# Kernel optimization log

Hardware: AMD Instinct MI355X
Metric: run time of the kernel (lower is better)

Reference implementation:

```python
import jax, jax.numpy as jnp
import numpy as np

HIDDEN = 128
NI = 100000   # ingredient nodes
NT = 100000   # taste nodes
E = 800000    # part_of edges
EPS = 1e-5


def setup_inputs() -> dict:
    key = jax.random.key(0)
    ks = jax.random.split(key, 12)
    s = 1.0 / np.sqrt(HIDDEN)
    return {
        "x_ingredient": jax.random.normal(ks[0], (NI, HIDDEN), jnp.float32),
        "x_taste": jax.random.normal(ks[1], (NT, HIDDEN), jnp.float32),
        "edge_index": jax.random.randint(ks[2], (2, E), 0, 100000, jnp.int64),
        "W_ing": jax.random.normal(ks[3], (HIDDEN, HIDDEN), jnp.float32) * s,
        "b_ing": jax.random.normal(ks[4], (HIDDEN,), jnp.float32) * s,
        "W_taste": jax.random.normal(ks[5], (HIDDEN, HIDDEN), jnp.float32) * s,
        "b_taste": jax.random.normal(ks[6], (HIDDEN,), jnp.float32) * s,
        "att_src": jax.random.normal(ks[7], (HIDDEN,), jnp.float32) * s,
        "att_dst": jax.random.normal(ks[8], (HIDDEN,), jnp.float32) * s,
        "k_lin_W": jax.random.normal(ks[9], (HIDDEN, HIDDEN), jnp.float32) * s,
        "k_lin_b": jax.random.normal(ks[10], (HIDDEN,), jnp.float32) * s,
        "q": jax.random.normal(ks[11], (HIDDEN,), jnp.float32) * s,
        "gamma": jnp.ones((HIDDEN,), jnp.float32),
        "beta": jnp.zeros((HIDDEN,), jnp.float32),
    }


def reference(x_ingredient, x_taste, edge_index, W_ing, b_ing, W_taste, b_taste,
              att_src, att_dst, k_lin_W, k_lin_b, q, gamma, beta):
    # Per-node-type linear projection (HANConv, heads=1)
    h_src = x_ingredient @ W_ing.T + b_ing      # [NI, D]
    h_dst = x_taste @ W_taste.T + b_taste       # [NT, D]

    # Per-node attention logits
    a_src = h_src @ att_src                     # [NI]
    a_dst = h_dst @ att_dst                     # [NT]

    src, dst = edge_index[0], edge_index[1]
    alpha = jax.nn.leaky_relu(a_src[src] + a_dst[dst], negative_slope=0.2)  # [E]

    # Segment softmax over incoming edges of each taste node
    m = jax.ops.segment_max(alpha, dst, num_segments=NT)
    m = jnp.where(jnp.isfinite(m), m, 0.0)      # empty segments -> 0
    e = jnp.exp(alpha - m[dst])
    denom = jax.ops.segment_sum(e, dst, num_segments=NT)
    coef = e / jnp.where(denom[dst] == 0, 1.0, denom[dst])  # [E]

    # Weighted scatter-add aggregation, then per-metapath ReLU (as in HANConv)
    agg = jax.ops.segment_sum(coef[:, None] * h_src[src], dst, num_segments=NT)  # [NT, D]
    agg = jax.nn.relu(agg)

    # Semantic attention across metapaths (single metapath -> weight 1.0)
    w = jnp.tanh(agg @ k_lin_W.T + k_lin_b).mean(0) @ q     # scalar
    beta_sem = jax.nn.softmax(w[None])[0]                   # == 1.0
    out = beta_sem * agg

    # BatchNorm (training statistics) + ReLU
    mu = out.mean(0)
    var = out.var(0)
    out = (out - mu) / jnp.sqrt(var + EPS) * gamma + beta
    return jax.nn.relu(out)
```

## Files before the change

kernel.cpp:

```cpp
#include <hip/hip_runtime.h>
#include <hip/hip_bf16.h>

#define HIDDEN 128
#define NI_N 100000
#define NT_N 100000
#define NE_N 800000
#define EPS_F 1e-5f
#define ELLW 32
#define STATS_B 512

#define NB_PROJ 782
#define NB_SC 512
#define SC_THREADS (NB_SC * 256)
#define SC_K 7
#define NB_ADST 3125
#define NB_ZERO 391

typedef __attribute__((ext_vector_type(8))) short bf16x8;
typedef __attribute__((ext_vector_type(4))) float f32x4;

static __device__ __forceinline__ unsigned short f2bf(float f) {
  unsigned u = __float_as_uint(f);
  u += 0x7FFFu + ((u >> 16) & 1u);
  return (unsigned short)(u >> 16);
}

static __device__ __forceinline__ bf16x8 pack8(float4 a, float4 b) {
  bf16x8 r;
  r[0] = (short)f2bf(a.x); r[1] = (short)f2bf(a.y);
  r[2] = (short)f2bf(a.z); r[3] = (short)f2bf(a.w);
  r[4] = (short)f2bf(b.x); r[5] = (short)f2bf(b.y);
  r[6] = (short)f2bf(b.z); r[7] = (short)f2bf(b.w);
  return r;
}

static __device__ __forceinline__ float bf_lo(unsigned int h) {
  return __uint_as_float(h << 16);
}
static __device__ __forceinline__ float bf_hi(unsigned int h) {
  return __uint_as_float(h & 0xffff0000u);
}


__global__ __launch_bounds__(256) void k_pre(const float* __restrict__ W,
                                             const float* __restrict__ b,
                                             const float* __restrict__ att,
                                             float* __restrict__ wbuf,
                                             int* __restrict__ cursor) {
  int bid = blockIdx.x, t = threadIdx.x;
  if (bid < NB_ZERO) {
    int i = bid * 256 + t;
    if (i < NT_N) cursor[i] = 0;
    return;
  }
  __shared__ float red[128];
  if (t < 128) {
    float s = 0.f;
#pragma unroll 8
    for (int c = 0; c < 128; ++c) s += att[c] * W[c * 128 + t];
    wbuf[t] = s;
    red[t] = att[t] * b[t];
  }
  __syncthreads();
  if (t < 64) {
    float v = red[t] + red[t + 64];
    v += __shfl_xor(v, 1);
    v += __shfl_xor(v, 2);
    v += __shfl_xor(v, 4);
    v += __shfl_xor(v, 8);
    v += __shfl_xor(v, 16);
    v += __shfl_xor(v, 32);
    if (t == 0) wbuf[128] = v;
  }
}

__global__ __launch_bounds__(256) void k_main(
    const float* __restrict__ x, const float* __restrict__ W,
    const float* __restrict__ bias, const float* __restrict__ att,
    unsigned int* __restrict__ h32, float* __restrict__ a_src,
    const int* __restrict__ esrc, const int* __restrict__ edst,
    int* __restrict__ cursor, int* __restrict__ ell,
    const float* __restrict__ xt, const float* __restrict__ wbuf,
    float* __restrict__ a_dst) {
  const int t = threadIdx.x;

  if (blockIdx.x >= NB_PROJ && blockIdx.x < NB_PROJ + NB_SC) {
    int base = (blockIdx.x - NB_PROJ) * 256 + t;
    int sv[SC_K], dv[SC_K];
    bool ok[SC_K];
#pragma unroll
    for (int k = 0; k < SC_K; ++k) {
      int e = base + k * SC_THREADS;
      ok[k] = e < NE_N;
      int ec = ok[k] ? e : (NE_N - 1);
      sv[k] = esrc[ec];
      dv[k] = edst[ec];
    }
#pragma unroll
    for (int k = 0; k < SC_K; ++k) {
      if (ok[k]) {
        int pos = atomicAdd(&cursor[dv[k]], 1);
        if (pos < ELLW) ell[dv[k] * ELLW + pos] = sv[k];
      }
    }
    return;
  }

  if (blockIdx.x >= NB_PROJ + NB_SC) {
    __shared__ float swe[128];
    if (t < 128) swe[t] = wbuf[t];
    __syncthreads();
    float be = wbuf[128];
    int lane = t & 63, wv = t >> 6;
    int sub = lane & 7, r = lane >> 3;
    int node = (blockIdx.x - NB_PROJ - NB_SC) * 32 + wv * 8 + r;
    if (node >= NT_N) return;
    const float* xp = xt + (size_t)node * 128 + sub * 4;
    float4 v0 = *(const float4*)(xp);
    float4 v1 = *(const float4*)(xp + 32);
    float4 v2 = *(const float4*)(xp + 64);
    float4 v3 = *(const float4*)(xp + 96);
    const float* wp = swe + sub * 4;
    float4 w0 = *(const float4*)(wp);
    float4 w1 = *(const float4*)(wp + 32);
    float4 w2 = *(const float4*)(wp + 64);
    float4 w3 = *(const float4*)(wp + 96);
    float s = v0.x * w0.x + v0.y * w0.y + v0.z * w0.z + v0.w * w0.w;
    s += v1.x * w1.x + v1.y * w1.y + v1.z * w1.z + v1.w * w1.w;
    s += v2.x * w2.x + v2.y * w2.y + v2.z * w2.z + v2.w * w2.w;
    s += v3.x * w3.x + v3.y * w3.y + v3.z * w3.z + v3.w * w3.w;
    s += __shfl_xor(s, 1);
    s += __shfl_xor(s, 2);
    s += __shfl_xor(s, 4);
    if (sub == 0) a_dst[node] = s + be;
    return;
  }

  const int bid = blockIdx.x;
  __shared__ float sh_a[128];
  if (t < 128) sh_a[t] = 0.f;
  __syncthreads();

  const int wave = t >> 6, lane = t & 63;
  const int colhalf = wave & 1, rowhalf = wave >> 1;
  const int row0 = bid * 128 + rowhalf * 64;
  const int lr = lane & 15;
  const int q = lane >> 4;

  bf16x8 bfrag[4][4];
  float bv[4], av[4];
#pragma unroll
  for (int nt = 0; nt < 4; ++nt) {
    int wrow = colhalf * 64 + nt * 16 + lr;
    const float* wp = W + wrow * 128 + q * 8;
#pragma unroll
    for (int kb = 0; kb < 4; ++kb) {
      float4 wa = *(const float4*)(wp + kb * 32);
      float4 wb = *(const float4*)(wp + kb * 32 + 4);
      bfrag[nt][kb] = pack8(wa, wb);
    }
    bv[nt] = bias[wrow];
    av[nt] = att[wrow];
  }

#pragma unroll
  for (int rt = 0; rt < 4; ++rt) {
    int arow = row0 + rt * 16 + lr;
    int rowc = (arow < NI_N) ? arow : (NI_N - 1);
    const float* xp = x + (size_t)rowc * 128 + q * 8;
    bf16x8 afrag[4];
#pragma unroll
    for (int kb = 0; kb < 4; ++kb) {
      float4 xa = *(const float4*)(xp + kb * 32);
      float4 xb = *(const float4*)(xp + kb * 32 + 4);
      afrag[kb] = pack8(xa, xb);
    }
    float part[4] = {0.f, 0.f, 0.f, 0.f};
    f32x4 cc[4];
#pragma unroll
    for (int nt = 0; nt < 4; ++nt) {
      f32x4 c = {0.f, 0.f, 0.f, 0.f};
#pragma unroll
      for (int kb = 0; kb < 4; ++kb)
        c = __builtin_amdgcn_mfma_f32_16x16x32_bf16(afrag[kb], bfrag[nt][kb], c,
                                                    0, 0, 0);
#pragma unroll
      for (int i = 0; i < 4; ++i) {
        float v = c[i] + bv[nt];
        part[i] += v * av[nt];
        c[i] = v;
      }
      cc[nt] = c;
    }
#pragma unroll
    for (int i = 0; i < 4; ++i) {
      int orow = row0 + rt * 16 + q * 4 + i;
      if (orow < NI_N) {
        unsigned u0 = (unsigned)f2bf(cc[0][i]) | ((unsigned)f2bf(cc[1][i]) << 16);
        unsigned u1 = (unsigned)f2bf(cc[2][i]) | ((unsigned)f2bf(cc[3][i]) << 16);
        unsigned int* hp = h32 + (size_t)orow * 64 + colhalf * 32 + lr;
        hp[0] = u0;
        hp[16] = u1;
      }
      float p = part[i];
      p += __shfl_xor(p, 1);
      p += __shfl_xor(p, 2);
      p += __shfl_xor(p, 4);
      p += __shfl_xor(p, 8);
      if (lr == 0)
        atomicAdd(&sh_a[rowhalf * 64 + rt * 16 + q * 4 + i], p);
    }
  }
  __syncthreads();
  if (t < 128) {
    int row = bid * 128 + t;
    if (row < NI_N) a_src[row] = sh_a[t];
  }
}

__global__ __launch_bounds__(256) void k_agg(const int* __restrict__ deg,
                                             const int* __restrict__ ell,
                                             const float* __restrict__ a_src,
                                             const float* __restrict__ a_dst,
                                             const unsigned int* __restrict__ h32,
                                             unsigned int* __restrict__ aggb) {
  int wv = (blockIdx.x * blockDim.x + threadIdx.x) >> 6;
  int lane = threadIdx.x & 63;
  int half = lane >> 5, l = lane & 31;
  int node = wv * 2 + half;
  if (node >= NT_N) return;
  int n = deg[node];
  n = (n > ELLW) ? ELLW : n;
  float ax = 0.f, ay = 0.f, bx = 0.f, by = 0.f;
  if (n > 0) {
    float ad = a_dst[node];
    int li = (l < n) ? l : (n - 1);
    int sr = ell[node * ELLW + li];
    float al = a_src[sr] + ad;
    al = (al > 0.f) ? al : 0.2f * al;
    float ex = (l < n) ? __expf(al) : 0.f;
    float den = 0.f;
    const int sb = half << 5;
    int n8 = (n + 7) & ~7;
    const uint2* h2 = (const uint2*)h32;
    for (int j = 0; j < n8; j += 8) {
      int s0 = __shfl(sr, sb + j + 0), s1 = __shfl(sr, sb + j + 1);
      int s2 = __shfl(sr, sb + j + 2), s3 = __shfl(sr, sb + j + 3);
      int s4 = __shfl(sr, sb + j + 4), s5 = __shfl(sr, sb + j + 5);
      int s6 = __shfl(sr, sb + j + 6), s7 = __shfl(sr, sb + j + 7);
      float e0 = __shfl(ex, sb + j + 0), e1 = __shfl(ex, sb + j + 1);
      float e2 = __shfl(ex, sb + j + 2), e3 = __shfl(ex, sb + j + 3);
      float e4 = __shfl(ex, sb + j + 4), e5 = __shfl(ex, sb + j + 5);
      float e6 = __shfl(ex, sb + j + 6), e7 = __shfl(ex, sb + j + 7);
      uint2 g0 = h2[s0 * 32 + l];
      uint2 g1 = h2[s1 * 32 + l];
      uint2 g2 = h2[s2 * 32 + l];
      uint2 g3 = h2[s3 * 32 + l];
      uint2 g4 = h2[s4 * 32 + l];
      uint2 g5 = h2[s5 * 32 + l];
      uint2 g6 = h2[s6 * 32 + l];
      uint2 g7 = h2[s7 * 32 + l];
      ax += e0 * bf_lo(g0.x) + e1 * bf_lo(g1.x) + e2 * bf_lo(g2.x) +
            e3 * bf_lo(g3.x) + e4 * bf_lo(g4.x) + e5 * bf_lo(g5.x) +
            e6 * bf_lo(g6.x) + e7 * bf_lo(g7.x);
      ay += e0 * bf_hi(g0.x) + e1 * bf_hi(g1.x) + e2 * bf_hi(g2.x) +
            e3 * bf_hi(g3.x) + e4 * bf_hi(g4.x) + e5 * bf_hi(g5.x) +
            e6 * bf_hi(g6.x) + e7 * bf_hi(g7.x);
      bx += e0 * bf_lo(g0.y) + e1 * bf_lo(g1.y) + e2 * bf_lo(g2.y) +
            e3 * bf_lo(g3.y) + e4 * bf_lo(g4.y) + e5 * bf_lo(g5.y) +
            e6 * bf_lo(g6.y) + e7 * bf_lo(g7.y);
      by += e0 * bf_hi(g0.y) + e1 * bf_hi(g1.y) + e2 * bf_hi(g2.y) +
            e3 * bf_hi(g3.y) + e4 * bf_hi(g4.y) + e5 * bf_hi(g5.y) +
            e6 * bf_hi(g6.y) + e7 * bf_hi(g7.y);
      den += ((e0 + e1) + (e2 + e3)) + ((e4 + e5) + (e6 + e7));
    }
    float inv = 1.f / den;
    ax *= inv; ay *= inv; bx *= inv; by *= inv;
  }
  ax = fmaxf(ax, 0.f);
  ay = fmaxf(ay, 0.f);
  bx = fmaxf(bx, 0.f);
  by = fmaxf(by, 0.f);
  uint2 o;
  o.x = (unsigned)f2bf(ax) | ((unsigned)f2bf(ay) << 16);
  o.y = (unsigned)f2bf(bx) | ((unsigned)f2bf(by) << 16);
  ((uint2*)aggb)[node * 32 + l] = o;
}

__global__ __launch_bounds__(256) void k_stats1(const unsigned int* __restrict__ aggb,
                                                float* __restrict__ partials) {
  __shared__ float red[4][64][4];
  int t = threadIdx.x;
  int p = t & 63, g = t >> 6;
  float sl = 0.f, ql = 0.f, sh_ = 0.f, qh = 0.f;
  for (int row = blockIdx.x * 4 + g; row < NT_N; row += STATS_B * 4) {
    unsigned int v = aggb[row * 64 + p];
    float lo = bf_lo(v), hi = bf_hi(v);
    sl += lo; ql += lo * lo;
    sh_ += hi; qh += hi * hi;
  }
  red[g][p][0] = sl; red[g][p][1] = ql;
  red[g][p][2] = sh_; red[g][p][3] = qh;
  __syncthreads();
  if (g == 0) {
    float4 v;
    v.x = red[0][p][0] + red[1][p][0] + red[2][p][0] + red[3][p][0];
    v.y = red[0][p][1] + red[1][p][1] + red[2][p][1] + red[3][p][1];
    v.z = red[0][p][2] + red[1][p][2] + red[2][p][2] + red[3][p][2];
    v.w = red[0][p][3] + red[1][p][3] + red[2][p][3] + red[3][p][3];
    ((float4*)partials)[blockIdx.x * 64 + p] = v;
  }
}

__global__ __launch_bounds__(256) void k_final2(const float* __restrict__ partials,
                                                const float* __restrict__ gamma,
                                                const float* __restrict__ beta,
                                                float* __restrict__ consts) {
  __shared__ float red[256];
  int e = threadIdx.x;
  float s = 0.f;
#pragma unroll 4
  for (int b = 0; b < STATS_B; ++b) s += partials[b * 256 + e];
  red[e] = s;
  __syncthreads();
  if (e < 128) {
    int c = e;
    int ch = c >> 6, rem = c & 63;
    int w = rem >> 5, rem2 = rem & 31;
    int half = rem2 >> 4, lr = rem2 & 15;
    int p = ch * 32 + w * 16 + lr;
    float sum = red[p * 4 + half * 2];
    float sq = red[p * 4 + half * 2 + 1];
    float mu = sum * (1.f / NT_N);
    float var = sq * (1.f / NT_N) - mu * mu;
    float sc = gamma[c] * rsqrtf(var + EPS_F);
    consts[c] = sc;
    consts[128 + c] = beta[c] - mu * sc;
  }
}

__global__ __launch_bounds__(256) void k_norm(const unsigned int* __restrict__ aggb,
                                              const float* __restrict__ consts,
                                              float* __restrict__ out) {
  int idx = blockIdx.x * 256 + threadIdx.x;
  if (idx >= NT_N * 64) return;
  int wid = idx >> 6, p = idx & 63;
  unsigned v = aggb[idx];
  float lo = bf_lo(v), hi = bf_hi(v);
  int c0 = (p >> 5) * 64 + ((p >> 4) & 1) * 32 + (p & 15);
  float r0 = fmaxf(lo * consts[c0] + consts[128 + c0], 0.f);
  float r1 = fmaxf(hi * consts[c0 + 16] + consts[144 + c0], 0.f);
  out[wid * 128 + c0] = r0;
  out[wid * 128 + c0 + 16] = r1;
}

extern "C" void kernel_launch(void* const* d_in, const int* in_sizes, int n_in,
                              void* d_out, int out_size, void* d_ws, size_t ws_size,
                              hipStream_t stream) {
  const float* x_ing = (const float*)d_in[0];
  const float* x_taste = (const float*)d_in[1];
  const int* edges = (const int*)d_in[2];
  const float* W_ing = (const float*)d_in[3];
  const float* b_ing = (const float*)d_in[4];
  const float* W_taste = (const float*)d_in[5];
  const float* b_taste = (const float*)d_in[6];
  const float* att_src = (const float*)d_in[7];
  const float* att_dst = (const float*)d_in[8];
  const float* gamma = (const float*)d_in[12];
  const float* beta = (const float*)d_in[13];
  float* out = (float*)d_out;
  (void)in_sizes; (void)n_in; (void)out_size; (void)ws_size;

  const int* e_src = edges;
  const int* e_dst = edges + NE_N;

  char* ws = (char*)d_ws;
  size_t off = 0;
  auto alloc = [&](size_t bytes) {
    void* p = ws + off;
    off += (bytes + 255) & ~size_t(255);
    return p;
  };
  unsigned int* h32 = (unsigned int*)alloc(sizeof(unsigned int) * NI_N * 64);
  unsigned int* aggb = (unsigned int*)alloc(sizeof(unsigned int) * NT_N * 64);
  float* a_src = (float*)alloc(sizeof(float) * NI_N);
  float* a_dst = (float*)alloc(sizeof(float) * NT_N);
  float* consts = (float*)alloc(sizeof(float) * 256);
  float* partials = (float*)alloc(sizeof(float) * STATS_B * 256);
  int* cursor = (int*)alloc(sizeof(int) * NT_N);
  int* ell = (int*)alloc(sizeof(int) * NT_N * ELLW);
  float* wbuf = (float*)alloc(sizeof(float) * 256);

  k_pre<<<NB_ZERO + 1, 256, 0, stream>>>(W_taste, b_taste, att_dst, wbuf,
                                         cursor);
  k_main<<<NB_PROJ + NB_SC + NB_ADST, 256, 0, stream>>>(
      x_ing, W_ing, b_ing, att_src, h32, a_src, e_src, e_dst, cursor, ell,
      x_taste, wbuf, a_dst);
  k_agg<<<((NT_N + 1) / 2 * 64 + 255) / 256, 256, 0, stream>>>(
      cursor, ell, a_src, a_dst, h32, aggb);
  k_stats1<<<STATS_B, 256, 0, stream>>>(aggb, partials);
  k_final2<<<1, 256, 0, stream>>>(partials, gamma, beta, consts);
  k_norm<<<(NT_N * 64 + 255) / 256, 256, 0, stream>>>(aggb, consts, out);
}
```

Baseline: 314.4 us.

## Fuse BN stats into aggregation, stage projection via LDS, vectorize norm, reorder blocks

Folds the batch-norm statistics pass into the aggregation kernel, which becomes a grid-stride kernel with per-block partials, so the separate stats read of aggb goes away. The projection path now loads x through double-buffered global_load_lds into swizzled shared memory, and its blocks are interleaved with the a_dst blocks. The normalize kernel is vectorized to uint4 loads and float4 stores, with the constants cached in LDS. The tradeoffs are larger LDS use in k_main (about 32KB for every block type, which can cut occupancy), extra barriers, and a larger final reduction over 1280 partials.

```diff
diff --git a/kernel.cpp b/kernel.cpp
--- a/kernel.cpp
+++ b/kernel.cpp
@@ -7,14 +7,15 @@
 #define NE_N 800000
 #define EPS_F 1e-5f
 #define ELLW 32
-#define STATS_B 512
 
 #define NB_PROJ 782
 #define NB_SC 512
 #define SC_THREADS (NB_SC * 256)
 #define SC_K 7
 #define NB_ADST 3125
+#define NB_MAIN (NB_SC + NB_PROJ + NB_ADST)
 #define NB_ZERO 391
+#define AGG_B 1280
 
 typedef __attribute__((ext_vector_type(8))) short bf16x8;
 typedef __attribute__((ext_vector_type(4))) float f32x4;
@@ -39,6 +40,12 @@
 }
 static __device__ __forceinline__ float bf_hi(unsigned int h) {
   return __uint_as_float(h & 0xffff0000u);
+}
+
+static __device__ __forceinline__ void gload_lds16(const float* g, float* l) {
+  __builtin_amdgcn_global_load_lds(
+      (const __attribute__((address_space(1))) unsigned int*)g,
+      (__attribute__((address_space(3))) unsigned int*)l, 16, 0, 0);
 }
 
 
@@ -83,9 +90,13 @@
     const float* __restrict__ xt, const float* __restrict__ wbuf,
     float* __restrict__ a_dst) {
   const int t = threadIdx.x;
-
-  if (blockIdx.x >= NB_PROJ && blockIdx.x < NB_PROJ + NB_SC) {
-    int base = (blockIdx.x - NB_PROJ) * 256 + t;
+  __shared__ float xs[2][32 * 128];
+  __shared__ float sh_a[128];
+  __shared__ float swe[128];
+
+  const int bx = blockIdx.x;
+  if (bx < NB_SC) {
+    int base = bx * 256 + t;
     int sv[SC_K], dv[SC_K];
     bool ok[SC_K];
 #pragma unroll
@@ -106,14 +117,15 @@
     return;
   }
 
-  if (blockIdx.x >= NB_PROJ + NB_SC) {
-    __shared__ float swe[128];
+  const int i = bx - NB_SC;
+  if (i % 5 != 0) {
+    int aid = i - (i + 4) / 5;
     if (t < 128) swe[t] = wbuf[t];
     __syncthreads();
     float be = wbuf[128];
     int lane = t & 63, wv = t >> 6;
     int sub = lane & 7, r = lane >> 3;
-    int node = (blockIdx.x - NB_PROJ - NB_SC) * 32 + wv * 8 + r;
+    int node = aid * 32 + wv * 8 + r;
     if (node >= NT_N) return;
     const float* xp = xt + (size_t)node * 128 + sub * 4;
     float4 v0 = *(const float4*)(xp);
@@ -136,10 +148,8 @@
     return;
   }
 
-  const int bid = blockIdx.x;
-  __shared__ float sh_a[128];
+  const int bid = i / 5;
   if (t < 128) sh_a[t] = 0.f;
-  __syncthreads();
 
   const int wave = t >> 6, lane = t & 63;
   const int colhalf = wave & 1, rowhalf = wave >> 1;
@@ -147,6 +157,19 @@
   const int lr = lane & 15;
   const int q = lane >> 4;
 
+  auto stage = [&](int rt, int b) {
+#pragma unroll
+    for (int j = 0; j < 4; ++j) {
+      int lrow = wave * 8 + j * 2 + (lane >> 5);
+      int strip = lrow >> 4, rr = lrow & 15;
+      int grow = bid * 128 + strip * 64 + rt * 16 + rr;
+      int rowc = (grow < NI_N) ? grow : (NI_N - 1);
+      int chunk = (lane & 31) ^ (lrow & 7);
+      gload_lds16(x + (size_t)rowc * 128 + chunk * 4,
+                  &xs[b][(wave * 8 + j * 2) * 128]);
+    }
+  };
+
   bf16x8 bfrag[4][4];
   float bv[4], av[4];
 #pragma unroll
@@ -163,16 +186,20 @@
     av[nt] = att[wrow];
   }
 
+  stage(0, 0);
+  __syncthreads();
+
 #pragma unroll
   for (int rt = 0; rt < 4; ++rt) {
-    int arow = row0 + rt * 16 + lr;
-    int rowc = (arow < NI_N) ? arow : (NI_N - 1);
-    const float* xp = x + (size_t)rowc * 128 + q * 8;
+    if (rt < 3) stage(rt + 1, (rt + 1) & 1);
+    const int lrow = rowhalf * 16 + lr;
+    const float* xrow = &xs[rt & 1][lrow * 128];
     bf16x8 afrag[4];
 #pragma unroll
     for (int kb = 0; kb < 4; ++kb) {
-      float4 xa = *(const float4*)(xp + kb * 32);
-      float4 xb = *(const float4*)(xp + kb * 32 + 4);
+      int c = kb * 8 + q * 2;
+      float4 xa = *(const float4*)(xrow + (c ^ (lrow & 7)) * 4);
+      float4 xb = *(const float4*)(xrow + ((c + 1) ^ (lrow & 7)) * 4);
       afrag[kb] = pack8(xa, xb);
     }
     float part[4] = {0.f, 0.f, 0.f, 0.f};
@@ -185,33 +212,33 @@
         c = __builtin_amdgcn_mfma_f32_16x16x32_bf16(afrag[kb], bfrag[nt][kb], c,
                                                     0, 0, 0);
 #pragma unroll
-      for (int i = 0; i < 4; ++i) {
-        float v = c[i] + bv[nt];
-        part[i] += v * av[nt];
-        c[i] = v;
+      for (int ii = 0; ii < 4; ++ii) {
+        float v = c[ii] + bv[nt];
+        part[ii] += v * av[nt];
+        c[ii] = v;
       }
       cc[nt] = c;
     }
 #pragma unroll
-    for (int i = 0; i < 4; ++i) {
-      int orow = row0 + rt * 16 + q * 4 + i;
+    for (int ii = 0; ii < 4; ++ii) {
+      int orow = row0 + rt * 16 + q * 4 + ii;
       if (orow < NI_N) {
-        unsigned u0 = (unsigned)f2bf(cc[0][i]) | ((unsigned)f2bf(cc[1][i]) << 16);
-        unsigned u1 = (unsigned)f2bf(cc[2][i]) | ((unsigned)f2bf(cc[3][i]) << 16);
+        unsigned u0 = (unsigned)f2bf(cc[0][ii]) | ((unsigned)f2bf(cc[1][ii]) << 16);
+        unsigned u1 = (unsigned)f2bf(cc[2][ii]) | ((unsigned)f2bf(cc[3][ii]) << 16);
         unsigned int* hp = h32 + (size_t)orow * 64 + colhalf * 32 + lr;
         hp[0] = u0;
         hp[16] = u1;
       }
-      float p = part[i];
+      float p = part[ii];
       p += __shfl_xor(p, 1);
       p += __shfl_xor(p, 2);
       p += __shfl_xor(p, 4);
       p += __shfl_xor(p, 8);
       if (lr == 0)
-        atomicAdd(&sh_a[rowhalf * 64 + rt * 16 + q * 4 + i], p);
-    }
-  }
-  __syncthreads();
+        atomicAdd(&sh_a[rowhalf * 64 + rt * 16 + q * 4 + ii], p);
+    }
+    __syncthreads();
+  }
   if (t < 128) {
     int row = bid * 128 + t;
     if (row < NI_N) a_src[row] = sh_a[t];
@@ -223,92 +250,87 @@
                                              const float* __restrict__ a_src,
                                              const float* __restrict__ a_dst,
                                              const unsigned int* __restrict__ h32,
-                                             unsigned int* __restrict__ aggb) {
-  int wv = (blockIdx.x * blockDim.x + threadIdx.x) >> 6;
-  int lane = threadIdx.x & 63;
-  int half = lane >> 5, l = lane & 31;
-  int node = wv * 2 + half;
-  if (node >= NT_N) return;
-  int n = deg[node];
-  n = (n > ELLW) ? ELLW : n;
-  float ax = 0.f, ay = 0.f, bx = 0.f, by = 0.f;
-  if (n > 0) {
-    float ad = a_dst[node];
-    int li = (l < n) ? l : (n - 1);
-    int sr = ell[node * ELLW + li];
-    float al = a_src[sr] + ad;
-    al = (al > 0.f) ? al : 0.2f * al;
-    float ex = (l < n) ? __expf(al) : 0.f;
-    float den = 0.f;
-    const int sb = half << 5;
-    int n8 = (n + 7) & ~7;
-    const uint2* h2 = (const uint2*)h32;
-    for (int j = 0; j < n8; j += 8) {
-      int s0 = __shfl(sr, sb + j + 0), s1 = __shfl(sr, sb + j + 1);
-      int s2 = __shfl(sr, sb + j + 2), s3 = __shfl(sr, sb + j + 3);
-      int s4 = __shfl(sr, sb + j + 4), s5 = __shfl(sr, sb + j + 5);
-      int s6 = __shfl(sr, sb + j + 6), s7 = __shfl(sr, sb + j + 7);
-      float e0 = __shfl(ex, sb + j + 0), e1 = __shfl(ex, sb + j + 1);
-      float e2 = __shfl(ex, sb + j + 2), e3 = __shfl(ex, sb + j + 3);
-      float e4 = __shfl(ex, sb + j + 4), e5 = __shfl(ex, sb + j + 5);
-      float e6 = __shfl(ex, sb + j + 6), e7 = __shfl(ex, sb + j + 7);
-      uint2 g0 = h2[s0 * 32 + l];
-      uint2 g1 = h2[s1 * 32 + l];
-      uint2 g2 = h2[s2 * 32 + l];
-      uint2 g3 = h2[s3 * 32 + l];
-      uint2 g4 = h2[s4 * 32 + l];
-      uint2 g5 = h2[s5 * 32 + l];
-      uint2 g6 = h2[s6 * 32 + l];
-      uint2 g7 = h2[s7 * 32 + l];
-      ax += e0 * bf_lo(g0.x) + e1 * bf_lo(g1.x) + e2 * bf_lo(g2.x) +
-            e3 * bf_lo(g3.x) + e4 * bf_lo(g4.x) + e5 * bf_lo(g5.x) +
-            e6 * bf_lo(g6.x) + e7 * bf_lo(g7.x);
-      ay += e0 * bf_hi(g0.x) + e1 * bf_hi(g1.x) + e2 * bf_hi(g2.x) +
-            e3 * bf_hi(g3.x) + e4 * bf_hi(g4.x) + e5 * bf_hi(g5.x) +
-            e6 * bf_hi(g6.x) + e7 * bf_hi(g7.x);
-      bx += e0 * bf_lo(g0.y) + e1 * bf_lo(g1.y) + e2 * bf_lo(g2.y) +
-            e3 * bf_lo(g3.y) + e4 * bf_lo(g4.y) + e5 * bf_lo(g5.y) +
-            e6 * bf_lo(g6.y) + e7 * bf_lo(g7.y);
-      by += e0 * bf_hi(g0.y) + e1 * bf_hi(g1.y) + e2 * bf_hi(g2.y) +
-            e3 * bf_hi(g3.y) + e4 * bf_hi(g4.y) + e5 * bf_hi(g5.y) +
-            e6 * bf_hi(g6.y) + e7 * bf_hi(g7.y);
-      den += ((e0 + e1) + (e2 + e3)) + ((e4 + e5) + (e6 + e7));
-    }
-    float inv = 1.f / den;
-    ax *= inv; ay *= inv; bx *= inv; by *= inv;
-  }
-  ax = fmaxf(ax, 0.f);
-  ay = fmaxf(ay, 0.f);
-  bx = fmaxf(bx, 0.f);
-  by = fmaxf(by, 0.f);
-  uint2 o;
-  o.x = (unsigned)f2bf(ax) | ((unsigned)f2bf(ay) << 16);
-  o.y = (unsigned)f2bf(bx) | ((unsigned)f2bf(by) << 16);
-  ((uint2*)aggb)[node * 32 + l] = o;
-}
-
-__global__ __launch_bounds__(256) void k_stats1(const unsigned int* __restrict__ aggb,
-                                                float* __restrict__ partials) {
-  __shared__ float red[4][64][4];
-  int t = threadIdx.x;
-  int p = t & 63, g = t >> 6;
-  float sl = 0.f, ql = 0.f, sh_ = 0.f, qh = 0.f;
-  for (int row = blockIdx.x * 4 + g; row < NT_N; row += STATS_B * 4) {
-    unsigned int v = aggb[row * 64 + p];
-    float lo = bf_lo(v), hi = bf_hi(v);
-    sl += lo; ql += lo * lo;
-    sh_ += hi; qh += hi * hi;
-  }
-  red[g][p][0] = sl; red[g][p][1] = ql;
-  red[g][p][2] = sh_; red[g][p][3] = qh;
+                                             unsigned int* __restrict__ aggb,
+                                             float* __restrict__ partials) {
+  const int t = threadIdx.x;
+  const int w = t >> 6, lane = t & 63;
+  const int half = lane >> 5, l = lane & 31;
+  const int sb = half << 5;
+  const uint2* h2 = (const uint2*)h32;
+  float st[8] = {0.f, 0.f, 0.f, 0.f, 0.f, 0.f, 0.f, 0.f};
+
+  for (int wv = blockIdx.x * 4 + w; wv < (NT_N + 1) / 2; wv += AGG_B * 4) {
+    int node = wv * 2 + half;
+    int n = deg[node];
+    n = (n > ELLW) ? ELLW : n;
+    float ax = 0.f, ay = 0.f, bx = 0.f, by = 0.f;
+    if (n > 0) {
+      float ad = a_dst[node];
+      int li = (l < n) ? l : (n - 1);
+      int sr = ell[node * ELLW + li];
+      float al = a_src[sr] + ad;
+      al = (al > 0.f) ? al : 0.2f * al;
+      float ex = (l < n) ? __expf(al) : 0.f;
+      float den = 0.f;
+      int n8 = (n + 7) & ~7;
+      for (int j = 0; j < n8; j += 8) {
+        int s0 = __shfl(sr, sb + j + 0), s1 = __shfl(sr, sb + j + 1);
+        int s2 = __shfl(sr, sb + j + 2), s3 = __shfl(sr, sb + j + 3);
+        int s4 = __shfl(sr, sb + j + 4), s5 = __shfl(sr, sb + j + 5);
+        int s6 = __shfl(sr, sb + j + 6), s7 = __shfl(sr, sb + j + 7);
+        float e0 = __shfl(ex, sb + j + 0), e1 = __shfl(ex, sb + j + 1);
+        float e2 = __shfl(ex, sb + j + 2), e3 = __shfl(ex, sb + j + 3);
+        float e4 = __shfl(ex, sb + j + 4), e5 = __shfl(ex, sb + j + 5);
+        float e6 = __shfl(ex, sb + j + 6), e7 = __shfl(ex, sb + j + 7);
+        uint2 g0 = h2[s0 * 32 + l];
+        uint2 g1 = h2[s1 * 32 + l];
+        uint2 g2 = h2[s2 * 32 + l];
+        uint2 g3 = h2[s3 * 32 + l];
+        uint2 g4 = h2[s4 * 32 + l];
+        uint2 g5 = h2[s5 * 32 + l];
+        uint2 g6 = h2[s6 * 32 + l];
+        uint2 g7 = h2[s7 * 32 + l];
+        ax += e0 * bf_lo(g0.x) + e1 * bf_lo(g1.x) + e2 * bf_lo(g2.x) +
+              e3 * bf_lo(g3.x) + e4 * bf_lo(g4.x) + e5 * bf_lo(g5.x) +
+              e6 * bf_lo(g6.x) + e7 * bf_lo(g7.x);
+        ay += e0 * bf_hi(g0.x) + e1 * bf_hi(g1.x) + e2 * bf_hi(g2.x) +
+              e3 * bf_hi(g3.x) + e4 * bf_hi(g4.x) + e5 * bf_hi(g5.x) +
+              e6 * bf_hi(g6.x) + e7 * bf_hi(g7.x);
+        bx += e0 * bf_lo(g0.y) + e1 * bf_lo(g1.y) + e2 * bf_lo(g2.y) +
+              e3 * bf_lo(g3.y) + e4 * bf_lo(g4.y) + e5 * bf_lo(g5.y) +
+              e6 * bf_lo(g6.y) + e7 * bf_lo(g7.y);
+        by += e0 * bf_hi(g0.y) + e1 * bf_hi(g1.y) + e2 * bf_hi(g2.y) +
+              e3 * bf_hi(g3.y) + e4 * bf_hi(g4.y) + e5 * bf_hi(g5.y) +
+              e6 * bf_hi(g6.y) + e7 * bf_hi(g7.y);
+        den += ((e0 + e1) + (e2 + e3)) + ((e4 + e5) + (e6 + e7));
+      }
+      float inv = 1.f / den;
+      ax *= inv; ay *= inv; bx *= inv; by *= inv;
+    }
+    ax = fmaxf(ax, 0.f);
+    ay = fmaxf(ay, 0.f);
+    bx = fmaxf(bx, 0.f);
+    by = fmaxf(by, 0.f);
+    uint2 o;
+    o.x = (unsigned)f2bf(ax) | ((unsigned)f2bf(ay) << 16);
+    o.y = (unsigned)f2bf(bx) | ((unsigned)f2bf(by) << 16);
+    ((uint2*)aggb)[node * 32 + l] = o;
+    st[0] += ax; st[1] += ax * ax; st[2] += ay; st[3] += ay * ay;
+    st[4] += bx; st[5] += bx * bx; st[6] += by; st[7] += by * by;
+  }
+
+  __shared__ float red[8][32][8];
+  int hw = w * 2 + half;
+#pragma unroll
+  for (int k = 0; k < 8; ++k) red[hw][l][k] = st[k];
   __syncthreads();
-  if (g == 0) {
-    float4 v;
-    v.x = red[0][p][0] + red[1][p][0] + red[2][p][0] + red[3][p][0];
-    v.y = red[0][p][1] + red[1][p][1] + red[2][p][1] + red[3][p][1];
-    v.z = red[0][p][2] + red[1][p][2] + red[2][p][2] + red[3][p][2];
-    v.w = red[0][p][3] + red[1][p][3] + red[2][p][3] + red[3][p][3];
-    ((float4*)partials)[blockIdx.x * 64 + p] = v;
+  {
+    int p = t >> 2, c = t & 3;
+    int l2 = p >> 1, u = p & 1;
+    float s = 0.f;
+#pragma unroll
+    for (int hw2 = 0; hw2 < 8; ++hw2) s += red[hw2][l2][u * 4 + c];
+    partials[blockIdx.x * 256 + t] = s;
   }
 }
 
@@ -320,7 +342,7 @@
   int e = threadIdx.x;
   float s = 0.f;
 #pragma unroll 4
-  for (int b = 0; b < STATS_B; ++b) s += partials[b * 256 + e];
+  for (int b = 0; b < AGG_B; ++b) s += partials[b * 256 + e];
   red[e] = s;
   __syncthreads();
   if (e < 128) {
@@ -342,16 +364,28 @@
 __global__ __launch_bounds__(256) void k_norm(const unsigned int* __restrict__ aggb,
                                               const float* __restrict__ consts,
                                               float* __restrict__ out) {
-  int idx = blockIdx.x * 256 + threadIdx.x;
-  if (idx >= NT_N * 64) return;
-  int wid = idx >> 6, p = idx & 63;
-  unsigned v = aggb[idx];
-  float lo = bf_lo(v), hi = bf_hi(v);
-  int c0 = (p >> 5) * 64 + ((p >> 4) & 1) * 32 + (p & 15);
-  float r0 = fmaxf(lo * consts[c0] + consts[128 + c0], 0.f);
-  float r1 = fmaxf(hi * consts[c0 + 16] + consts[144 + c0], 0.f);
-  out[wid * 128 + c0] = r0;
-  out[wid * 128 + c0 + 16] = r1;
+  __shared__ float sc[256];
+  int t = threadIdx.x;
+  sc[t] = consts[t];
+  __syncthreads();
+  int u = blockIdx.x * 256 + t;
+  if (u >= NT_N * 16) return;
+  uint4 v = ((const uint4*)aggb)[u];
+  int wid = u >> 4, k = u & 15;
+  int p0 = k * 4;
+  int c0 = (p0 >> 5) * 64 + ((p0 >> 4) & 1) * 32 + (p0 & 15);
+  unsigned vv[4] = {v.x, v.y, v.z, v.w};
+  float o0[4], o1[4];
+#pragma unroll
+  for (int j = 0; j < 4; ++j) {
+    int c = c0 + j;
+    float lo = bf_lo(vv[j]), hi = bf_hi(vv[j]);
+    o0[j] = fmaxf(lo * sc[c] + sc[128 + c], 0.f);
+    o1[j] = fmaxf(hi * sc[c + 16] + sc[144 + c], 0.f);
+  }
+  float* op = out + (size_t)wid * 128 + c0;
+  *(float4*)op = make_float4(o0[0], o0[1], o0[2], o0[3]);
+  *(float4*)(op + 16) = make_float4(o1[0], o1[1], o1[2], o1[3]);
 }
 
 extern "C" void kernel_launch(void* const* d_in, const int* in_sizes, int n_in,
@@ -386,19 +420,18 @@
   float* a_src = (float*)alloc(sizeof(float) * NI_N);
   float* a_dst = (float*)alloc(sizeof(float) * NT_N);
   float* consts = (float*)alloc(sizeof(float) * 256);
-  float* partials = (float*)alloc(sizeof(float) * STATS_B * 256);
+  float* partials = (float*)alloc(sizeof(float) * AGG_B * 256);
   int* cursor = (int*)alloc(sizeof(int) * NT_N);
   int* ell = (int*)alloc(sizeof(int) * NT_N * ELLW);
   float* wbuf = (float*)alloc(sizeof(float) * 256);
 
   k_pre<<<NB_ZERO + 1, 256, 0, stream>>>(W_taste, b_taste, att_dst, wbuf,
                                          cursor);
-  k_main<<<NB_PROJ + NB_SC + NB_ADST, 256, 0, stream>>>(
+  k_main<<<NB_MAIN, 256, 0, stream>>>(
       x_ing, W_ing, b_ing, att_src, h32, a_src, e_src, e_dst, cursor, ell,
       x_taste, wbuf, a_dst);
-  k_agg<<<((NT_N + 1) / 2 * 64 + 255) / 256, 256, 0, stream>>>(
-      cursor, ell, a_src, a_dst, h32, aggb);
-  k_stats1<<<STATS_B, 256, 0, stream>>>(aggb, partials);
+  k_agg<<<AGG_B, 256, 0, stream>>>(cursor, ell, a_src, a_dst, h32, aggb,
+                                   partials);
   k_final2<<<1, 256, 0, stream>>>(partials, gamma, beta, consts);
-  k_norm<<<(NT_N * 64 + 255) / 256, 256, 0, stream>>>(aggb, consts, out);
-}
+  k_norm<<<(NT_N * 16 + 255) / 256, 256, 0, stream>>>(aggb, consts, out);
+}
```

After: 399.7 us. +27.1%, slower.
